# Kernel tuning notes

Measured on AMD Instinct MI355X. Metric: run time of the kernel, lower is better.

## Reference

```python
import jax, jax.numpy as jnp
import numpy as np

H = 256
N0, N1, N2 = 150000, 80000, 20000
E0, E1 = 800000, 300000


def setup_inputs() -> dict:
    key = jax.random.key(0)
    ks = jax.random.split(key, 16)
    sc = 1.0 / np.sqrt(H)
    return {
        "x": jax.random.normal(ks[0], (N0, H), jnp.float32),
        # GATConv params (heads=1): lin weight, att_src, att_dst, bias
        "W_gat": jax.random.normal(ks[1], (H, H), jnp.float32) * sc,
        "att_src": jax.random.normal(ks[2], (H,), jnp.float32) * sc,
        "att_dst": jax.random.normal(ks[3], (H,), jnp.float32) * sc,
        "b_gat": jax.random.normal(ks[4], (H,), jnp.float32) * 0.01,
        # SAGEConv layer 0: lin_l (aggregated, with bias), lin_r (root, no bias)
        "Wl0": jax.random.normal(ks[5], (H, H), jnp.float32) * sc,
        "bl0": jnp.zeros((H,), jnp.float32),
        "Wr0": jax.random.normal(ks[6], (H, H), jnp.float32) * sc,
        # SAGEConv layer 1
        "Wl1": jax.random.normal(ks[7], (H, H), jnp.float32) * sc,
        "bl1": jnp.zeros((H,), jnp.float32),
        "Wr1": jax.random.normal(ks[8], (H, H), jnp.float32) * sc,
        # NeighborSampler bipartite edge lists (src -> dst)
        "src0": jax.random.randint(ks[9], (E0,), 0, N0, dtype=jnp.int32),
        "dst0": jax.random.randint(ks[10], (E0,), 0, N1, dtype=jnp.int32),
        "src1": jax.random.randint(ks[11], (E1,), 0, N1, dtype=jnp.int32),
        "dst1": jax.random.randint(ks[12], (E1,), 0, N2, dtype=jnp.int32),
        "n1": N1,
        "n2": N2,
    }


def _gat(x, src, dst, W, a_s, a_d, b):
    """PyG GATConv, heads=1, add_self_loops=True, eval mode (dropout no-op)."""
    N = x.shape[0]
    h = x @ W                                   # [N, H]
    loops = jnp.arange(N, dtype=src.dtype)      # self loops over all N nodes
    s = jnp.concatenate([src, loops])
    d = jnp.concatenate([dst, loops])
    al_s = (h * a_s).sum(-1)                    # [N]
    al_d = (h * a_d).sum(-1)                    # [N]
    e = jax.nn.leaky_relu(al_s[s] + al_d[d], 0.2)
    m = jax.ops.segment_max(e, d, num_segments=N)     # softmax over dst groups
    w = jnp.exp(e - m[d])
    z = jax.ops.segment_sum(w, d, num_segments=N)
    coef = w / z[d]
    out = jax.ops.segment_sum(coef[:, None] * h[s], d, num_segments=N)
    return out + b


def _sage(x_src, x_tgt, src, dst, n_tgt, Wl, bl, Wr):
    """PyG SAGEConv((x, x_target), edge_index), mean aggr, normalize=True."""
    msg = x_src[src]                                         # [E, H]
    ssum = jax.ops.segment_sum(msg, dst, num_segments=n_tgt)
    cnt = jax.ops.segment_sum(jnp.ones(src.shape, msg.dtype), dst,
                              num_segments=n_tgt)
    mean = ssum / jnp.maximum(cnt, 1.0)[:, None]
    out = mean @ Wl + bl + x_tgt @ Wr
    nrm = jnp.linalg.norm(out, axis=-1, keepdims=True)       # F.normalize
    return out / jnp.maximum(nrm, 1e-12)


def reference(x, W_gat, att_src, att_dst, b_gat, Wl0, bl0, Wr0, Wl1, bl1, Wr1,
              src0, dst0, src1, dst1, n1, n2):
    # Layer 0 (its result is discarded by the original module: x = x_all each
    # iteration and only the final x is appended to xs).
    h0 = _gat(x, src0, dst0, W_gat, att_src, att_dst, b_gat)
    _ = jax.nn.relu(_sage(h0, h0[:n1], src0, dst0, n1, Wl0, bl0, Wr0))
    # Layer 1 (the returned output)
    h1 = _gat(x, src1, dst1, W_gat, att_src, att_dst, b_gat)
    out = _sage(h1, h1[:n2], src1, dst1, n2, Wl1, bl1, Wr1)
    return out
```

## Files before the change

kernel.cpp:

```cpp
#include <hip/hip_runtime.h>


#define NS 80000
#define ND 20000

typedef float   float4v  __attribute__((ext_vector_type(4)));
typedef float   f32x4    __attribute__((ext_vector_type(4)));
typedef __bf16  bf16x8   __attribute__((ext_vector_type(8)));
typedef unsigned short ushort8v __attribute__((ext_vector_type(8)));
typedef unsigned short ushort2v __attribute__((ext_vector_type(2)));
typedef int     int4v    __attribute__((ext_vector_type(4)));

union frag_u { ushort8v u; bf16x8 b; };

__device__ __forceinline__ float us2f(unsigned short u) {
    union { unsigned int i; float f; } x; x.i = ((unsigned)u) << 16; return x.f;
}
__device__ __forceinline__ unsigned short f2us(float f) {
    union { __bf16 b; unsigned short u; } x; x.b = (__bf16)f; return x.u;
}
__device__ __forceinline__ float lrelu02(float x) { return x > 0.f ? x : 0.2f * x; }

__global__ __launch_bounds__(256) void prep_misc(
    const float* __restrict__ Wg, const float* __restrict__ Wl,
    const float* __restrict__ Wr, unsigned short* __restrict__ Wgp,
    unsigned short* __restrict__ Wcp, int* __restrict__ zerop, int nz4)
{
    const int b = blockIdx.x, t = threadIdx.x;
    if (b < 256) {
        const int n = b;
        const int k = t;
        Wgp[(((k >> 3) * 256) + n) * 8 + (k & 7)] = f2us(Wg[k * 256 + n]);
    } else if (b < 512) {
        const int n = b - 256;
        const int k0 = t;
        const int k1 = t + 256;
        Wcp[(((k0 >> 3) * 256) + n) * 8 + (k0 & 7)] = f2us(Wl[t * 256 + n]);
        Wcp[(((k1 >> 3) * 256) + n) * 8 + (k1 & 7)] = f2us(Wr[t * 256 + n]);
    } else {
        const int i = (b - 512) * 256 + t;
        if (i < nz4) ((int4v*)zerop)[i] = (int4v){0, 0, 0, 0};
    }
}

__global__ void count_rank(const int* __restrict__ src, const int* __restrict__ dst,
                           int* __restrict__ cntpair, int* __restrict__ rank, int E)
{
    const int i = blockIdx.x * 256 + threadIdx.x;
    if (i < E) {
        const int d = dst[i];
        const int cls = (src[i] < ND) ? 0 : 1;
        rank[i] = atomicAdd(&cntpair[2 * d + cls], 1);
    }
}

template <int EPI, bool AF32, bool SCAN, int KC>
__global__ __launch_bounds__(512) void gemm_mfma(
    const void* __restrict__ Av, const unsigned short* __restrict__ Bp,
    int M,
    unsigned short* __restrict__ hb_out,
    const float* __restrict__ avs, const float* __restrict__ avd,
    float* __restrict__ al_s, float* __restrict__ al_d,
    const float* __restrict__ bias, float* __restrict__ outp,
    int nblk, const int* __restrict__ cntpair, int* __restrict__ ptrp)
{
    __shared__ __align__(16) unsigned short Als[2][128][40];
    __shared__ float red0[128];
    __shared__ float red1[128];
    __shared__ int   part[512];

    if (SCAN && (int)blockIdx.x >= nblk) {
        const int tid = threadIdx.x;
        const int chunk = (ND + 511) / 512;
        const int i0 = tid * chunk;
        const int i1 = min(i0 + chunk, ND);
        int s = 0;
        for (int i = i0; i < i1; ++i) s += cntpair[2*i] + cntpair[2*i+1];
        part[tid] = s;
        __syncthreads();
        for (int off = 1; off < 512; off <<= 1) {
            const int t = (tid >= off) ? part[tid - off] : 0;
            __syncthreads();
            part[tid] += t;
            __syncthreads();
        }
        int run = tid ? part[tid - 1] : 0;
        for (int i = i0; i < i1; ++i) { ptrp[i] = run; run += cntpair[2*i] + cntpair[2*i+1]; }
        if (tid == 511) ptrp[ND] = part[511];
        return;
    }

    const int tid  = threadIdx.x;
    const int lane = tid & 63;
    const int wid  = tid >> 6;
    const int wr   = wid >> 2;
    const int wc   = wid & 3;
    const int row0 = blockIdx.x * 128;
    const int lg   = lane >> 4;
    const int lm   = lane & 15;

    f32x4 acc[4][4] = {};
    constexpr int nk = KC >> 5;

    const int arow = tid >> 2;
    const int akof = (tid & 3) * 8;

    float4v ar0, ar1;
    ushort8v ai;

    auto loadA = [&](int kt) {
        const int k0 = kt * 32 + akof;
        const int grow = row0 + arow;
        if constexpr (AF32) {
            const float* p = (const float*)Av + (size_t)grow * KC + k0;
            ar0 = *(const float4v*)p;
            ar1 = *(const float4v*)(p + 4);
        } else {
            if (grow < M)
                ai = *(const ushort8v*)((const unsigned short*)Av + (size_t)grow * KC + k0);
            else
                ai = (ushort8v){0,0,0,0,0,0,0,0};
        }
    };
    auto storeA = [&](int b) {
        if constexpr (AF32) {
            ushort8v t;
            t[0] = f2us(ar0[0]); t[1] = f2us(ar0[1]); t[2] = f2us(ar0[2]); t[3] = f2us(ar0[3]);
            t[4] = f2us(ar1[0]); t[5] = f2us(ar1[1]); t[6] = f2us(ar1[2]); t[7] = f2us(ar1[3]);
            *(ushort8v*)&Als[b][arow][akof] = t;
        } else {
            *(ushort8v*)&Als[b][arow][akof] = ai;
        }
    };

    loadA(0); storeA(0); __syncthreads();
    int cur = 0;

#pragma unroll
    for (int kt = 0; kt < nk; ++kt) {
        if (kt + 1 < nk) loadA(kt + 1);
        frag_u bf[4];
#pragma unroll
        for (int n = 0; n < 4; ++n)
            bf[n].u = *(const ushort8v*)(Bp +
                ((size_t)(kt*4 + lg) * 256 + wc*64 + n*16 + lm) * 8);
        frag_u af[4];
#pragma unroll
        for (int m = 0; m < 4; ++m)
            af[m].u = *(const ushort8v*)&Als[cur][wr*64 + m*16 + lm][lg*8];
#pragma unroll
        for (int m = 0; m < 4; ++m)
#pragma unroll
            for (int n = 0; n < 4; ++n)
                acc[m][n] = __builtin_amdgcn_mfma_f32_16x16x32_bf16(
                    af[m].b, bf[n].b, acc[m][n], 0, 0, 0);
        if (kt + 1 < nk) {
            storeA(cur ^ 1);
            __syncthreads();
            cur ^= 1;
        }
    }

    if constexpr (EPI == 0) {
        if (tid < 128) { red0[tid] = 0.f; red1[tid] = 0.f; }
        __syncthreads();
        float asv[4], adv[4], bgv[4];
#pragma unroll
        for (int n = 0; n < 4; ++n) {
            const int col = wc*64 + n*16 + lm;
            asv[n] = avs[col]; adv[n] = avd[col]; bgv[n] = bias[col];
        }
#pragma unroll
        for (int m = 0; m < 4; ++m) {
#pragma unroll
            for (int j = 0; j < 4; ++j) {
                const int lr = wr*64 + m*16 + lg*4 + j;
                float ps = 0.f, pd = 0.f;
#pragma unroll
                for (int n = 0; n < 4; ++n) {
                    const float v = acc[m][n][j];
                    ps += v * asv[n]; pd += v * adv[n];
                    hb_out[(size_t)(row0 + lr) * 256 + wc*64 + n*16 + lm] = f2us(v + bgv[n]);
                }
#pragma unroll
                for (int off = 1; off < 16; off <<= 1) {
                    ps += __shfl_xor(ps, off);
                    pd += __shfl_xor(pd, off);
                }
                if (lm == 0) { atomicAdd(&red0[lr], ps); atomicAdd(&red1[lr], pd); }
            }
        }
        __syncthreads();
        if (tid < 128) { al_s[row0 + tid] = red0[tid]; al_d[row0 + tid] = red1[tid]; }
    } else {
        if (tid < 128) red0[tid] = 0.f;
        __syncthreads();
        float bv[4];
#pragma unroll
        for (int n = 0; n < 4; ++n) bv[n] = bias[wc*64 + n*16 + lm];
#pragma unroll
        for (int m = 0; m < 4; ++m) {
#pragma unroll
            for (int j = 0; j < 4; ++j) {
                const int lr = wr*64 + m*16 + lg*4 + j;
                float ss = 0.f;
#pragma unroll
                for (int n = 0; n < 4; ++n) {
                    const float v = acc[m][n][j] + bv[n];
                    acc[m][n][j] = v;
                    ss += v * v;
                }
#pragma unroll
                for (int off = 1; off < 16; off <<= 1) ss += __shfl_xor(ss, off);
                if (lm == 0) atomicAdd(&red0[lr], ss);
            }
        }
        __syncthreads();
#pragma unroll
        for (int m = 0; m < 4; ++m) {
#pragma unroll
            for (int j = 0; j < 4; ++j) {
                const int lr = wr*64 + m*16 + lg*4 + j;
                const int grow = row0 + lr;
                if (grow < M) {
                    const float inv = 1.0f / fmaxf(sqrtf(red0[lr]), 1e-12f);
#pragma unroll
                    for (int n = 0; n < 4; ++n)
                        outp[(size_t)grow * 256 + wc*64 + n*16 + lm] = acc[m][n][j] * inv;
                }
            }
        }
    }
}

__global__ void edge_scatter(const int* __restrict__ src, const int* __restrict__ dst,
                             const int* __restrict__ ptrp, const int* __restrict__ rank,
                             const int* __restrict__ cntpair,
                             int* __restrict__ ssort, int E)
{
    const int i = blockIdx.x * 256 + threadIdx.x;
    if (i < E) {
        const int d = dst[i];
        const int s = src[i];
        const int base = ptrp[d];
        const int pos = (s < ND) ? base + rank[i]
                                 : base + cntpair[2 * d] + rank[i];
        ssort[pos] = s;
    }
}

__global__ __launch_bounds__(256) void gat_sage(
    const unsigned short* __restrict__ hb, const float* __restrict__ al_s,
    const float* __restrict__ al_d, const int* __restrict__ ssort,
    const int* __restrict__ ptrp, unsigned short* __restrict__ hcat)
{
    __shared__ float ldsg[2][4][264];
    __shared__ float ldss[2][4][264];
    __shared__ float zp[2][4];
    const int tid  = threadIdx.x;
    const int grp  = tid >> 7;
    const int t    = tid & 127;
    const int slot = t >> 5;
    const int l32  = t & 31;
    const int c0   = l32 * 8;
    const int v    = blockIdx.x * 2 + grp;
    const int p0 = ptrp[v], p1 = ptrp[v + 1];

    const float ad     = al_d[v];
    const float w_self = __expf(lrelu02(al_s[v] + ad));

    float accg[8], accs[8];
    float zpart = 0.f;
#pragma unroll
    for (int j = 0; j < 8; ++j) accs[j] = 0.f;
    if (slot == 0) {
        const ushort8v hv = *(const ushort8v*)&hb[(size_t)v * 256 + c0];
#pragma unroll
        for (int j = 0; j < 8; ++j) accg[j] = w_self * us2f(hv[j]);
    } else {
#pragma unroll
        for (int j = 0; j < 8; ++j) accg[j] = 0.f;
    }

    int p = p0 + slot;
    for (; p + 4 < p1; p += 8) {
        const int s0 = ssort[p];
        const int s1 = ssort[p + 4];
        const float w0 = __expf(lrelu02(al_s[s0] + ad));
        const float w1 = __expf(lrelu02(al_s[s1] + ad));
        const ushort8v h0 = *(const ushort8v*)&hb[(size_t)s0 * 256 + c0];
        const ushort8v h1 = *(const ushort8v*)&hb[(size_t)s1 * 256 + c0];
        zpart += w0 + w1;
        const bool g0 = (s0 >= ND), g1 = (s1 >= ND);
#pragma unroll
        for (int j = 0; j < 8; ++j) {
            const float f0 = us2f(h0[j]);
            const float f1 = us2f(h1[j]);
            accg[j] = fmaf(w0, f0, accg[j]);
            accg[j] = fmaf(w1, f1, accg[j]);
            accs[j] += (g0 ? f0 : 0.f) + (g1 ? f1 : 0.f);
        }
    }
    if (p < p1) {
        const int s0 = ssort[p];
        const float w0 = __expf(lrelu02(al_s[s0] + ad));
        const ushort8v h0 = *(const ushort8v*)&hb[(size_t)s0 * 256 + c0];
        zpart += w0;
        const bool g0 = (s0 >= ND);
#pragma unroll
        for (int j = 0; j < 8; ++j) {
            const float f0 = us2f(h0[j]);
            accg[j] = fmaf(w0, f0, accg[j]);
            accs[j] += g0 ? f0 : 0.f;
        }
    }

    if (l32 == 0) zp[grp][slot] = zpart;
    *(f32x4*)&ldsg[grp][slot][c0]     = (f32x4){accg[0], accg[1], accg[2], accg[3]};
    *(f32x4*)&ldsg[grp][slot][c0 + 4] = (f32x4){accg[4], accg[5], accg[6], accg[7]};
    *(f32x4*)&ldss[grp][slot][c0]     = (f32x4){accs[0], accs[1], accs[2], accs[3]};
    *(f32x4*)&ldss[grp][slot][c0 + 4] = (f32x4){accs[4], accs[5], accs[6], accs[7]};
    __syncthreads();

    const float inv_z = 1.0f / (w_self + zp[grp][0] + zp[grp][1] + zp[grp][2] + zp[grp][3]);
    const int c = t * 2;
    float rg0 = 0.f, rg1 = 0.f, rs0 = 0.f, rs1 = 0.f;
#pragma unroll
    for (int s2 = 0; s2 < 4; ++s2) {
        rg0 += ldsg[grp][s2][c];     rg1 += ldsg[grp][s2][c + 1];
        rs0 += ldss[grp][s2][c];     rs1 += ldss[grp][s2][c + 1];
    }
    *(ushort2v*)&hcat[(size_t)v * 512 + 256 + c] =
        (ushort2v){f2us(rg0 * inv_z), f2us(rg1 * inv_z)};
    *(ushort2v*)&hcat[(size_t)v * 512 + c] =
        (ushort2v){f2us(rs0), f2us(rs1)};
}

__global__ __launch_bounds__(256) void sage_fin(
    const int* __restrict__ ssort, const int* __restrict__ ptrp,
    const int* __restrict__ cntpair, unsigned short* __restrict__ hcat)
{
    const int tid   = threadIdx.x;
    const int g     = tid >> 6;
    const int v     = blockIdx.x * 4 + g;
    const int slot2 = (tid >> 5) & 1;
    const int l32   = tid & 31;
    const int c0    = l32 * 8;
    const int p0  = ptrp[v];
    const int p1l = p0 + cntpair[2 * v];
    const int deg = ptrp[v + 1] - p0;

    float acc[8];
    if (slot2 == 0) {
        const ushort8v pv = *(const ushort8v*)&hcat[(size_t)v * 512 + c0];
#pragma unroll
        for (int j = 0; j < 8; ++j) acc[j] = us2f(pv[j]);
    } else {
#pragma unroll
        for (int j = 0; j < 8; ++j) acc[j] = 0.f;
    }
    int p = p0 + slot2;
    for (; p + 2 < p1l; p += 4) {
        const int s0 = ssort[p];
        const int s1 = ssort[p + 2];
        const ushort8v h0 = *(const ushort8v*)&hcat[(size_t)s0 * 512 + 256 + c0];
        const ushort8v h1 = *(const ushort8v*)&hcat[(size_t)s1 * 512 + 256 + c0];
#pragma unroll
        for (int j = 0; j < 8; ++j) acc[j] += us2f(h0[j]) + us2f(h1[j]);
    }
    if (p < p1l) {
        const int s0 = ssort[p];
        const ushort8v h0 = *(const ushort8v*)&hcat[(size_t)s0 * 512 + 256 + c0];
#pragma unroll
        for (int j = 0; j < 8; ++j) acc[j] += us2f(h0[j]);
    }
#pragma unroll
    for (int j = 0; j < 8; ++j) acc[j] += __shfl_xor(acc[j], 32);

    const float inv = (deg > 0) ? 1.0f / (float)deg : 0.f;
    if (slot2 == 0) {
        ushort8v o;
#pragma unroll
        for (int j = 0; j < 8; ++j) o[j] = f2us(acc[j] * inv);
        *(ushort8v*)&hcat[(size_t)v * 512 + c0] = o;
    }
}

extern "C" void kernel_launch(void* const* d_in, const int* in_sizes, int n_in,
                              void* d_out, int out_size, void* d_ws, size_t ws_size,
                              hipStream_t stream)
{
    const float* x    = (const float*)d_in[0];
    const float* Wg   = (const float*)d_in[1];
    const float* asrc = (const float*)d_in[2];
    const float* adst = (const float*)d_in[3];
    const float* bg   = (const float*)d_in[4];
    const float* Wl1  = (const float*)d_in[8];
    const float* bl1  = (const float*)d_in[9];
    const float* Wr1  = (const float*)d_in[10];
    const int*   src1 = (const int*)d_in[13];
    const int*   dst1 = (const int*)d_in[14];
    const int E1 = in_sizes[13];

    char* w = (char*)d_ws;
    unsigned short* hb   = (unsigned short*)w; w += (size_t)NS * 256 * 2;
    unsigned short* hcat = (unsigned short*)w; w += (size_t)ND * 512 * 2;
    unsigned short* Wgp  = (unsigned short*)w; w += 256 * 256 * 2;
    unsigned short* Wcp  = (unsigned short*)w; w += 256 * 512 * 2;
    float* al_s   = (float*)w; w += (size_t)NS * 4;
    float* al_d   = (float*)w; w += (size_t)NS * 4;
    int* cntpair  = (int*)w;   w += (size_t)2 * ND * 4;
    int* ptrv     = (int*)w;   w += (size_t)(ND + 4) * 4;
    int* rank     = (int*)w;   w += (size_t)E1 * 4;
    int* ssort    = (int*)w;   w += (size_t)E1 * 4;

    const dim3 b256(256), b512(512);
    const int nz4 = 2 * ND / 4;

    prep_misc<<<dim3(512 + (nz4 + 255) / 256), b256, 0, stream>>>(
        Wg, Wl1, Wr1, Wgp, Wcp, cntpair, nz4);

    count_rank<<<dim3((E1 + 255) / 256), b256, 0, stream>>>(
        src1, dst1, cntpair, rank, E1);

    const int nblk0 = NS / 128;
    gemm_mfma<0, true, true, 256><<<dim3(nblk0 + 1), b512, 0, stream>>>(
        x, Wgp, NS, hb, asrc, adst, al_s, al_d, bg, nullptr,
        nblk0, cntpair, ptrv);

    edge_scatter<<<dim3((E1 + 255) / 256), b256, 0, stream>>>(
        src1, dst1, ptrv, rank, cntpair, ssort, E1);

    gat_sage<<<dim3(ND / 2), b256, 0, stream>>>(hb, al_s, al_d, ssort,
                                                ptrv, hcat);
    sage_fin<<<dim3(ND / 4), b256, 0, stream>>>(ssort, ptrv, cntpair, hcat);

    gemm_mfma<1, false, false, 512><<<dim3((ND + 127) / 128), b512, 0, stream>>>(
        hcat, Wcp, ND, nullptr, nullptr, nullptr, nullptr, nullptr,
        bl1, (float*)d_out, 0, nullptr, nullptr);
}
```

Before: 147.6 us.

## Fuse edge counting into GEMM launch and shrink final GEMM row tile

```diff
diff --git a/kernel.cpp b/kernel.cpp
--- a/kernel.cpp
+++ b/kernel.cpp
@@ -43,18 +43,7 @@
     }
 }
 
-__global__ void count_rank(const int* __restrict__ src, const int* __restrict__ dst,
-                           int* __restrict__ cntpair, int* __restrict__ rank, int E)
-{
-    const int i = blockIdx.x * 256 + threadIdx.x;
-    if (i < E) {
-        const int d = dst[i];
-        const int cls = (src[i] < ND) ? 0 : 1;
-        rank[i] = atomicAdd(&cntpair[2 * d + cls], 1);
-    }
-}
-
-template <int EPI, bool AF32, bool SCAN, int KC>
+template <int EPI, bool AF32, bool SCAN, int KC, int TM>
 __global__ __launch_bounds__(512) void gemm_mfma(
     const void* __restrict__ Av, const unsigned short* __restrict__ Bp,
     int M,
@@ -62,15 +51,33 @@
     const float* __restrict__ avs, const float* __restrict__ avd,
     float* __restrict__ al_s, float* __restrict__ al_d,
     const float* __restrict__ bias, float* __restrict__ outp,
-    int nblk, const int* __restrict__ cntpair, int* __restrict__ ptrp)
-{
-    __shared__ __align__(16) unsigned short Als[2][128][40];
+    int nblk, int* __restrict__ cntpair, int* __restrict__ ptrp,
+    const int* __restrict__ srcE, const int* __restrict__ dstE,
+    int* __restrict__ rank, int E, int* __restrict__ done_ctr, int ncnt)
+{
+    __shared__ __align__(16) unsigned short Als[2][TM][40];
     __shared__ float red0[128];
     __shared__ float red1[128];
     __shared__ int   part[512];
 
-    if (SCAN && (int)blockIdx.x >= nblk) {
+    if (SCAN && (int)blockIdx.x > nblk) {
+        const int i = ((int)blockIdx.x - nblk - 1) * 512 + (int)threadIdx.x;
+        if (i < E) {
+            const int d = dstE[i];
+            const int cls = (srcE[i] < ND) ? 0 : 1;
+            rank[i] = atomicAdd(&cntpair[2 * d + cls], 1);
+        }
+        __syncthreads();
+        __threadfence();
+        if (threadIdx.x == 0) atomicAdd(done_ctr, 1);
+        return;
+    }
+    if (SCAN && (int)blockIdx.x == nblk) {
         const int tid = threadIdx.x;
+        if (tid == 0) {
+            while (atomicAdd(done_ctr, 0) < ncnt) { __builtin_amdgcn_s_sleep(8); }
+        }
+        __syncthreads();
         const int chunk = (ND + 511) / 512;
         const int i0 = tid * chunk;
         const int i1 = min(i0 + chunk, ND);
@@ -93,9 +100,9 @@
     const int tid  = threadIdx.x;
     const int lane = tid & 63;
     const int wid  = tid >> 6;
-    const int wr   = wid >> 2;
-    const int wc   = wid & 3;
-    const int row0 = blockIdx.x * 128;
+    const int wr   = (TM == 128) ? (wid >> 2) : 0;
+    const int wc   = (TM == 128) ? (wid & 3) : wid;
+    const int row0 = blockIdx.x * TM;
     const int lg   = lane >> 4;
     const int lm   = lane & 15;
 
@@ -162,7 +169,7 @@
     }
 
     if constexpr (EPI == 0) {
-        if (tid < 128) { red0[tid] = 0.f; red1[tid] = 0.f; }
+        if (tid < TM) { red0[tid] = 0.f; red1[tid] = 0.f; }
         __syncthreads();
         float asv[4], adv[4], bgv[4];
 #pragma unroll
@@ -191,9 +198,9 @@
             }
         }
         __syncthreads();
-        if (tid < 128) { al_s[row0 + tid] = red0[tid]; al_d[row0 + tid] = red1[tid]; }
+        if (tid < TM) { al_s[row0 + tid] = red0[tid]; al_d[row0 + tid] = red1[tid]; }
     } else {
-        if (tid < 128) red0[tid] = 0.f;
+        if (tid < TM) red0[tid] = 0.f;
         __syncthreads();
         float bv[4];
 #pragma unroll
@@ -410,23 +417,22 @@
     float* al_s   = (float*)w; w += (size_t)NS * 4;
     float* al_d   = (float*)w; w += (size_t)NS * 4;
     int* cntpair  = (int*)w;   w += (size_t)2 * ND * 4;
+    int* done     = (int*)w;   w += 4 * 4;
     int* ptrv     = (int*)w;   w += (size_t)(ND + 4) * 4;
     int* rank     = (int*)w;   w += (size_t)E1 * 4;
     int* ssort    = (int*)w;   w += (size_t)E1 * 4;
 
     const dim3 b256(256), b512(512);
-    const int nz4 = 2 * ND / 4;
+    const int nz4 = (2 * ND + 4) / 4;
 
     prep_misc<<<dim3(512 + (nz4 + 255) / 256), b256, 0, stream>>>(
         Wg, Wl1, Wr1, Wgp, Wcp, cntpair, nz4);
 
-    count_rank<<<dim3((E1 + 255) / 256), b256, 0, stream>>>(
-        src1, dst1, cntpair, rank, E1);
-
     const int nblk0 = NS / 128;
-    gemm_mfma<0, true, true, 256><<<dim3(nblk0 + 1), b512, 0, stream>>>(
+    const int ncnt  = (E1 + 511) / 512;
+    gemm_mfma<0, true, true, 256, 128><<<dim3(nblk0 + 1 + ncnt), b512, 0, stream>>>(
         x, Wgp, NS, hb, asrc, adst, al_s, al_d, bg, nullptr,
-        nblk0, cntpair, ptrv);
+        nblk0, cntpair, ptrv, src1, dst1, rank, E1, done, ncnt);
 
     edge_scatter<<<dim3((E1 + 255) / 256), b256, 0, stream>>>(
         src1, dst1, ptrv, rank, cntpair, ssort, E1);
@@ -435,7 +441,8 @@
                                                 ptrv, hcat);
     sage_fin<<<dim3(ND / 4), b256, 0, stream>>>(ssort, ptrv, cntpair, hcat);
 
-    gemm_mfma<1, false, false, 512><<<dim3((ND + 127) / 128), b512, 0, stream>>>(
+    gemm_mfma<1, false, false, 512, 64><<<dim3((ND + 63) / 64), b256, 0, stream>>>(
         hcat, Wcp, ND, nullptr, nullptr, nullptr, nullptr, nullptr,
-        bl1, (float*)d_out, 0, nullptr, nullptr);
-}
+        bl1, (float*)d_out, 0, nullptr, nullptr, nullptr, nullptr,
+        nullptr, 0, nullptr, 0);
+}
```

Measured after the change: 275.0 us. 1.86x slower.
